# Kernel optimization log

Hardware: AMD Instinct MI355X
Metric: run time of the kernel (lower is better)

## Reference

```python
import jax, jax.numpy as jnp
import numpy as np

NHEAD = 16
HEAD_DIM = 64
ROPE_BASE = 10000.0


def _rotate_half(x):
    # interleaved convention: pairs (x0,x1)->(-x1,x0)
    x1 = x[..., ::2]
    x2 = x[..., 1::2]
    return jnp.stack([-x2, x1], axis=-1).reshape(x.shape)


def _rope_cache(seq_len, head_dim, base):
    half = head_dim // 2
    inv_freq = 1.0 / base ** (jnp.arange(half, dtype=jnp.float32) / float(half))
    t = jnp.arange(seq_len, dtype=jnp.float32)
    freqs = jnp.einsum('i,j->ij', t, inv_freq)          # [T, half]
    emb = jnp.concatenate([freqs, freqs], axis=-1)      # [T, D] (half-half cat, matches torch source)
    return jnp.cos(emb), jnp.sin(emb)


def setup_inputs() -> dict:
    key = jax.random.key(0)
    k1, k2, k3 = jax.random.split(key, 3)
    b, t, c = 2, 2048, 1024
    x = jax.random.normal(k1, (b, t, c), dtype=jnp.float32)
    # torch nn.Linear weights: [out_features, in_features], scaled like kaiming-uniform-ish
    W_qkv = jax.random.normal(k2, (3 * c, c), dtype=jnp.float32) / np.sqrt(c)
    W_out = jax.random.normal(k3, (c, c), dtype=jnp.float32) / np.sqrt(c)
    return {"x": x, "W_qkv": W_qkv, "W_out": W_out}


def reference(x, W_qkv, W_out):
    b, t, c = x.shape
    nh, hd = NHEAD, HEAD_DIM
    qkv = x @ W_qkv.T                                   # [b, t, 3c]
    q, k, v = jnp.split(qkv, 3, axis=-1)

    def to_heads(a):
        return a.reshape(b, t, nh, hd).transpose(0, 2, 1, 3)  # [b, nh, t, hd]

    q, k, v = to_heads(q), to_heads(k), to_heads(v)
    cos, sin = _rope_cache(t, hd, ROPE_BASE)            # [t, hd]
    cos = cos.astype(q.dtype)[None, None]
    sin = sin.astype(q.dtype)[None, None]
    q = q * cos + _rotate_half(q) * sin
    k = k * cos + _rotate_half(k) * sin

    scale = 1.0 / np.sqrt(hd).astype(np.float32)
    scores = jnp.einsum('bhqd,bhkd->bhqk', q, k) * scale
    attn = jax.nn.softmax(scores, axis=-1)
    y = jnp.einsum('bhqk,bhkd->bhqd', attn, v)          # [b, nh, t, hd]
    y = y.transpose(0, 2, 1, 3).reshape(b, t, c)
    return y @ W_out.T
```

## Files before the change

kernel.cpp:

```cpp
#include <hip/hip_runtime.h>
#include <hip/hip_bf16.h>
#include <math.h>

typedef __hip_bfloat16 bf16;
typedef _Float16 f16;
typedef __attribute__((ext_vector_type(8))) short bf16x8;
typedef __attribute__((ext_vector_type(8))) _Float16 f16x8;
typedef __attribute__((ext_vector_type(4))) float f32x4;
typedef __attribute__((ext_vector_type(4))) unsigned u32x4;

#define MFMA_BF(a,b,c) __builtin_amdgcn_mfma_f32_16x16x32_bf16((a),(b),(c),0,0,0)
#define MFMA_F16(a,b,c) __builtin_amdgcn_mfma_f32_16x16x32_f16((a),(b),(c),0,0,0)

__device__ __forceinline__ void load_lds16(const void* g, void* l) {
  __builtin_amdgcn_global_load_lds(
      (__attribute__((address_space(1))) void*)(g),
      (__attribute__((address_space(3))) void*)(l), 16, 0, 0);
}

__device__ __forceinline__ unsigned pk_bf16(float a, float b) {
  unsigned ua = __builtin_bit_cast(unsigned, a);
  unsigned ub = __builtin_bit_cast(unsigned, b);
  ua += 0x7fffu + ((ua >> 16) & 1u);
  ub += 0x7fffu + ((ub >> 16) & 1u);
  return (ua >> 16) | (ub & 0xffff0000u);
}

__device__ __forceinline__ unsigned cvtpk_bf16(float a, float b) {
  unsigned r;
  __asm__("v_cvt_pk_bf16_f32 %0, %1, %2" : "=v"(r) : "v"(a), "v"(b));
  return r;
}

__global__ void cvt_all(const float* __restrict__ x, const float* __restrict__ wq,
                        const float* __restrict__ wo, unsigned* __restrict__ xb,
                        unsigned* __restrict__ wqb, unsigned* __restrict__ wob) {
  int i = blockIdx.x * blockDim.x + threadIdx.x;
  const float* src;
  unsigned* dst;
  int off;
  if (i < 1048576) { src = x; dst = xb; off = i; }
  else if (i < 1048576 + 786432) { src = wq; dst = wqb; off = i - 1048576; }
  else { src = wo; dst = wob; off = i - (1048576 + 786432); }
  float4 v = reinterpret_cast<const float4*>(src)[off];
  uint2 u;
  u.x = cvtpk_bf16(v.x, v.y);
  u.y = cvtpk_bf16(v.z, v.w);
  reinterpret_cast<uint2*>(dst)[off] = u;
}

__global__ __launch_bounds__(256, 3)
void gemm_qkv(const bf16* __restrict__ A, const bf16* __restrict__ B,
              bf16* __restrict__ outq, bf16* __restrict__ outk,
              f16* __restrict__ outv) {
  __shared__ __align__(16) bf16 As[3][128 * 32];
  __shared__ __align__(16) bf16 Bs[3][128 * 32];
  const int K = 1024;
  const int tid = threadIdx.x;
  const int w = tid >> 6;
  const int lane = tid & 63;
  const int quad = lane >> 4;
  const int col = lane & 15;
  const int waveM = w >> 1;
  const int waveN = w & 1;
  const int bm = blockIdx.y * 128;
  const int bn = blockIdx.x * 128;

  f32x4 acc[4][4] = {};
  const int srow = lane >> 2;
  const int skoff = (((lane & 3) ^ ((srow >> 1) & 3))) * 8;
  const int swq = (quad ^ ((col >> 1) & 3)) * 8;

  auto stage = [&](int k0, int sb) {
#pragma unroll
    for (int p = 0; p < 2; ++p) {
      int r = p * 64 + w * 16 + srow;
      load_lds16(A + (size_t)(bm + r) * K + k0 + skoff,
                 (char*)As + sb * 8192 + p * 4096 + w * 1024);
      load_lds16(B + (size_t)(bn + r) * K + k0 + skoff,
                 (char*)Bs + sb * 8192 + p * 4096 + w * 1024);
    }
  };

  stage(0, 0);
  stage(32, 1);

  int cb = 0;
  for (int k0 = 0; k0 < K; k0 += 32) {
    if (k0 + 32 < K) __asm__ volatile("s_waitcnt vmcnt(4)" ::: "memory");
    else             __asm__ volatile("s_waitcnt vmcnt(0)" ::: "memory");
    __asm__ volatile("s_barrier" ::: "memory");
    if (k0 + 64 < K) {
      int nb = cb + 2; if (nb >= 3) nb -= 3;
      stage(k0 + 64, nb);
    }
    const bf16* at = &As[cb][0];
    const bf16* bt = &Bs[cb][0];
    bf16x8 af[4], bfr[4];
#pragma unroll
    for (int i = 0; i < 4; ++i)
      af[i] = *reinterpret_cast<const bf16x8*>(at + (waveM * 64 + i * 16 + col) * 32 + swq);
#pragma unroll
    for (int j = 0; j < 4; ++j)
      bfr[j] = *reinterpret_cast<const bf16x8*>(bt + (waveN * 64 + j * 16 + col) * 32 + swq);
#pragma unroll
    for (int i = 0; i < 4; ++i)
#pragma unroll
      for (int j = 0; j < 4; ++j)
        acc[i][j] = MFMA_BF(af[i], bfr[j], acc[i][j]);
    cb = (cb == 2) ? 0 : cb + 1;
  }

  if (bn < 2048) {
    const float NEGK = -0.4152410118f;
    const float C1 = 0.1803368799f;
    const float sgn = (col & 1) ? 1.0f : -1.0f;
#pragma unroll
    for (int j = 0; j < 4; ++j) {
      const int n0 = bn + waveN * 64 + j * 16;
      const int sel = n0 >> 10;
      const int hh = (n0 & 1023) >> 6;
      const int dd = (n0 & 63) + col;
      bf16* outp = sel ? outk : outq;
      const float post = sel ? 1.0f : C1;
      const float invf = __builtin_amdgcn_exp2f((float)((n0 & 31) + col) * NEGK);
#pragma unroll
      for (int i = 0; i < 4; ++i) {
#pragma unroll
        for (int r = 0; r < 4; ++r) {
          int m = bm + waveM * 64 + i * 16 + quad * 4 + r;
          int b = m >> 11, t = m & 2047;
          float v = acc[i][j][r];
          float partner = __shfl_xor(v, 1);
          float ang = (float)t * invf;
          float res = (v * __cosf(ang) + sgn * partner * __sinf(ang)) * post;
          outp[((size_t)(b * 16 + hh) * 2048 + t) * 64 + dd] = __float2bfloat16(res);
        }
      }
    }
  } else {
    const int b = bm >> 11;
    const int tt0 = (bm & 2047) + waveM * 64;
#pragma unroll
    for (int j = 0; j < 4; ++j) {
      const int n0 = bn + waveN * 64 + j * 16;
      const int hh = (n0 & 1023) >> 6;
      const int dd = (n0 & 63) + col;
      f16* dst = outv + (size_t)(b * 16 + hh) * 131072 + (size_t)dd * 2048;
#pragma unroll
      for (int i = 0; i < 4; ++i) {
        uint2 pk;
        pk.x = __builtin_bit_cast(unsigned, __builtin_amdgcn_cvt_pkrtz(acc[i][j][0], acc[i][j][1]));
        pk.y = __builtin_bit_cast(unsigned, __builtin_amdgcn_cvt_pkrtz(acc[i][j][2], acc[i][j][3]));
        *reinterpret_cast<uint2*>(dst + tt0 + i * 16 + quad * 4) = pk;
      }
    }
  }
}

__global__ __launch_bounds__(256, 4)
void gemm_out(const bf16* __restrict__ A, const bf16* __restrict__ B,
              float* __restrict__ outf) {
  __shared__ __align__(16) bf16 As[3][64 * 32];
  __shared__ __align__(16) bf16 Bs[3][64 * 32];
  const int K = 1024;
  const int tid = threadIdx.x;
  const int w = tid >> 6;
  const int lane = tid & 63;
  const int quad = lane >> 4;
  const int col = lane & 15;
  const int waveM = w >> 1;
  const int waveN = w & 1;
  const int bm = blockIdx.y * 64;
  const int bn = blockIdx.x * 64;

  f32x4 acc[2][2] = {};
  const int srow = lane >> 2;
  const int skoff = (((lane & 3) ^ ((srow >> 1) & 3))) * 8;
  const int swq = (quad ^ ((col >> 1) & 3)) * 8;

  auto stage = [&](int k0, int sb) {
    int r = w * 16 + srow;
    load_lds16(A + (size_t)(bm + r) * K + k0 + skoff,
               (char*)As + sb * 4096 + w * 1024);
    load_lds16(B + (size_t)(bn + r) * K + k0 + skoff,
               (char*)Bs + sb * 4096 + w * 1024);
  };

  stage(0, 0);
  stage(32, 1);

  int cb = 0;
  for (int k0 = 0; k0 < K; k0 += 32) {
    if (k0 + 32 < K) __asm__ volatile("s_waitcnt vmcnt(2)" ::: "memory");
    else             __asm__ volatile("s_waitcnt vmcnt(0)" ::: "memory");
    __asm__ volatile("s_barrier" ::: "memory");
    if (k0 + 64 < K) {
      int nb = cb + 2; if (nb >= 3) nb -= 3;
      stage(k0 + 64, nb);
    }
    const bf16* at = &As[cb][0];
    const bf16* bt = &Bs[cb][0];
    bf16x8 af[2], bfr[2];
#pragma unroll
    for (int i = 0; i < 2; ++i)
      af[i] = *reinterpret_cast<const bf16x8*>(at + (waveM * 32 + i * 16 + col) * 32 + swq);
#pragma unroll
    for (int j = 0; j < 2; ++j)
      bfr[j] = *reinterpret_cast<const bf16x8*>(bt + (waveN * 32 + j * 16 + col) * 32 + swq);
#pragma unroll
    for (int i = 0; i < 2; ++i)
#pragma unroll
      for (int j = 0; j < 2; ++j)
        acc[i][j] = MFMA_BF(af[i], bfr[j], acc[i][j]);
    cb = (cb == 2) ? 0 : cb + 1;
  }

#pragma unroll
  for (int i = 0; i < 2; ++i)
#pragma unroll
    for (int j = 0; j < 2; ++j) {
      const int n0 = bn + waveN * 32 + j * 16;
#pragma unroll
      for (int r = 0; r < 4; ++r) {
        int m = bm + waveM * 32 + i * 16 + quad * 4 + r;
        outf[(size_t)m * 1024 + n0 + col] = acc[i][j][r];
      }
    }
}

__global__ __launch_bounds__(256, 2)
void attn_kernel(const bf16* __restrict__ qh, const bf16* __restrict__ kh,
                 const f16* __restrict__ vt, bf16* __restrict__ y) {
  __shared__ __align__(16) bf16 Ks[2][2 * 64 * 64];
  __shared__ __align__(16) f16 Vs[3][2 * 64 * 64];

  const int bh = blockIdx.x;
  const int qt = blockIdx.y;
  const int w = threadIdx.x >> 6;
  const int lane = threadIdx.x & 63;
  const int quad = lane >> 4;
  const int col = lane & 15;

  const int qrow0 = qt * 128 + w * 32 + col;
  bf16x8 qf[2][2];
#pragma unroll
  for (int f = 0; f < 2; ++f)
#pragma unroll
    for (int c = 0; c < 2; ++c)
      qf[f][c] = *reinterpret_cast<const bf16x8*>(
          qh + ((size_t)bh * 2048 + qrow0 + f * 16) * 64 + c * 32 + quad * 8);

  const int s8 = lane >> 3;
  const int blk = (lane & 7) ^ s8;
  const bf16* kg = kh + (size_t)bh * 2048 * 64;
  const f16* vg = vt + (size_t)bh * 64 * 2048;
  const int ks0 = 32 * (w >> 1) + 8 * ((4 * w + (s8 >> 2)) & 3) + 4 * (w & 1) + (s8 & 3);
  const int ks1 = 32 * (w >> 1) + 8 * ((4 * w + 2 + (s8 >> 2)) & 3) + 4 * (w & 1) + (s8 & 3);
  const int vrow0 = w * 16 + s8;

  const int csw = col & 7;
  const int sw0 = (quad ^ csw) * 8;
  const int sw1 = ((quad + 4) ^ csw) * 8;
  const int rdbase = col * 64;

  f32x4 O[2][4] = {};
  float l[2] = {};
  f16x8 pf[2][4];

  auto stageK2 = [&](int kn, int kb) {
    char* kbp = (char*)Ks + kb * 16384 + w * 2048;
    load_lds16(kg + (size_t)(kn + ks0) * 64 + blk * 8, kbp);
    load_lds16(kg + (size_t)(kn + ks1) * 64 + blk * 8, kbp + 1024);
    load_lds16(kg + (size_t)(kn + 64 + ks0) * 64 + blk * 8, kbp + 8192);
    load_lds16(kg + (size_t)(kn + 64 + ks1) * 64 + blk * 8, kbp + 8192 + 1024);
  };
  auto stageV2 = [&](int kn, int vb) {
    char* vbp = (char*)Vs + vb * 16384 + w * 2048;
    load_lds16(vg + (size_t)vrow0 * 2048 + kn + blk * 8, vbp);
    load_lds16(vg + (size_t)(vrow0 + 8) * 2048 + kn + blk * 8, vbp + 1024);
    load_lds16(vg + (size_t)vrow0 * 2048 + kn + 64 + blk * 8, vbp + 8192);
    load_lds16(vg + (size_t)(vrow0 + 8) * 2048 + kn + 64 + blk * 8, vbp + 8192 + 1024);
  };

  auto softmax = [&](f32x4 (&s)[2][2][4]) {
#pragma unroll
    for (int f = 0; f < 2; ++f) {
      unsigned pk[16];
      float lf = 0.0f;
#pragma unroll
      for (int u = 0; u < 2; ++u)
#pragma unroll
        for (int t = 0; t < 4; ++t) {
          float p0 = __builtin_amdgcn_exp2f(s[f][u][t][0]);
          float p1 = __builtin_amdgcn_exp2f(s[f][u][t][1]);
          float p2 = __builtin_amdgcn_exp2f(s[f][u][t][2]);
          float p3 = __builtin_amdgcn_exp2f(s[f][u][t][3]);
          lf += (p0 + p1) + (p2 + p3);
          pk[u * 8 + t * 2]     = __builtin_bit_cast(unsigned, __builtin_amdgcn_cvt_pkrtz(p0, p1));
          pk[u * 8 + t * 2 + 1] = __builtin_bit_cast(unsigned, __builtin_amdgcn_cvt_pkrtz(p2, p3));
        }
      l[f] += lf;
      pf[f][0] = __builtin_bit_cast(f16x8, (u32x4){pk[0], pk[1], pk[2], pk[3]});
      pf[f][1] = __builtin_bit_cast(f16x8, (u32x4){pk[4], pk[5], pk[6], pk[7]});
      pf[f][2] = __builtin_bit_cast(f16x8, (u32x4){pk[8], pk[9], pk[10], pk[11]});
      pf[f][3] = __builtin_bit_cast(f16x8, (u32x4){pk[12], pk[13], pk[14], pk[15]});
    }
  };

  stageK2(0, 0);
  stageV2(0, 0);

  __asm__ volatile("s_waitcnt vmcnt(4)" ::: "memory");
  __asm__ volatile("s_barrier" ::: "memory");
  stageK2(128, 1);
  stageV2(128, 1);
  {
    f32x4 s[2][2][4];
    __builtin_amdgcn_s_setprio(1);
#pragma unroll
    for (int u = 0; u < 2; ++u) {
      const bf16* kt = &Ks[0][u * 4096];
#pragma unroll
      for (int t = 0; t < 4; ++t) {
        bf16x8 kf0 = *reinterpret_cast<const bf16x8*>(kt + t * 1024 + rdbase + sw0);
        bf16x8 kf1 = *reinterpret_cast<const bf16x8*>(kt + t * 1024 + rdbase + sw1);
#pragma unroll
        for (int f = 0; f < 2; ++f) {
          f32x4 a = {};
          a = MFMA_BF(kf0, qf[f][0], a);
          a = MFMA_BF(kf1, qf[f][1], a);
          s[f][u][t] = a;
        }
      }
    }
    __builtin_amdgcn_s_setprio(0);
    softmax(s);
  }

  int vprev = 0;
  int vnext = 2;
#pragma unroll 1
  for (int c = 1; c < 16; ++c) {
    const int kc = c * 128;
    __asm__ volatile("s_waitcnt vmcnt(4)" ::: "memory");
    __asm__ volatile("s_barrier" ::: "memory");
    if (c + 1 < 16) {
      stageK2(kc + 128, (c + 1) & 1);
      stageV2(kc + 128, vnext);
    }

    f32x4 s[2][2][4];
    __builtin_amdgcn_s_setprio(1);
#pragma unroll
    for (int u = 0; u < 2; ++u) {
      const bf16* kt = &Ks[c & 1][u * 4096];
      const f16* vtile = &Vs[vprev][u * 4096];
#pragma unroll
      for (int t = 0; t < 4; ++t) {
        bf16x8 kf0 = *reinterpret_cast<const bf16x8*>(kt + t * 1024 + rdbase + sw0);
        bf16x8 kf1 = *reinterpret_cast<const bf16x8*>(kt + t * 1024 + rdbase + sw1);
        f16x8 vf0 = *reinterpret_cast<const f16x8*>(vtile + t * 1024 + rdbase + sw0);
        f16x8 vf1 = *reinterpret_cast<const f16x8*>(vtile + t * 1024 + rdbase + sw1);
#pragma unroll
        for (int f = 0; f < 2; ++f) {
          f32x4 a = {};
          a = MFMA_BF(kf0, qf[f][0], a);
          a = MFMA_BF(kf1, qf[f][1], a);
          s[f][u][t] = a;
          O[f][t] = MFMA_F16(vf0, pf[f][u * 2], O[f][t]);
          O[f][t] = MFMA_F16(vf1, pf[f][u * 2 + 1], O[f][t]);
        }
      }
    }
    __builtin_amdgcn_s_setprio(0);
    softmax(s);

    vprev = (vprev == 2) ? 0 : vprev + 1;
    vnext = (vnext == 2) ? 0 : vnext + 1;
  }

  __asm__ volatile("s_waitcnt vmcnt(0)" ::: "memory");
  __asm__ volatile("s_barrier" ::: "memory");
  {
    __builtin_amdgcn_s_setprio(1);
#pragma unroll
    for (int u = 0; u < 2; ++u) {
      const f16* vtile = &Vs[vprev][u * 4096];
#pragma unroll
      for (int t = 0; t < 4; ++t) {
        f16x8 vf0 = *reinterpret_cast<const f16x8*>(vtile + t * 1024 + rdbase + sw0);
        f16x8 vf1 = *reinterpret_cast<const f16x8*>(vtile + t * 1024 + rdbase + sw1);
#pragma unroll
        for (int f = 0; f < 2; ++f) {
          O[f][t] = MFMA_F16(vf0, pf[f][u * 2], O[f][t]);
          O[f][t] = MFMA_F16(vf1, pf[f][u * 2 + 1], O[f][t]);
        }
      }
    }
    __builtin_amdgcn_s_setprio(0);
  }

  const int b = bh >> 4, h = bh & 15;
#pragma unroll
  for (int f = 0; f < 2; ++f) {
    float lv = l[f];
    lv += __shfl_xor(lv, 16, 64);
    lv += __shfl_xor(lv, 32, 64);
    float inv = 1.0f / lv;
    int tq = qt * 128 + w * 32 + f * 16 + col;
    size_t base = ((size_t)b * 2048 + tq) * 1024 + h * 64;
#pragma unroll
    for (int j = 0; j < 4; ++j) {
      uint2 pk2;
      pk2.x = pk_bf16(O[f][j][0] * inv, O[f][j][1] * inv);
      pk2.y = pk_bf16(O[f][j][2] * inv, O[f][j][3] * inv);
      *reinterpret_cast<uint2*>((unsigned short*)y + base + j * 16 + quad * 4) = pk2;
    }
  }
}

extern "C" void kernel_launch(void* const* d_in, const int* in_sizes, int n_in,
                              void* d_out, int out_size, void* d_ws, size_t ws_size,
                              hipStream_t stream) {
  const float* x    = (const float*)d_in[0];
  const float* wqkv = (const float*)d_in[1];
  const float* wout = (const float*)d_in[2];
  float* out = (float*)d_out;
  char* ws = (char*)d_ws;

  bf16* xb    = (bf16*)(ws);
  bf16* wqkvb = (bf16*)(ws + (size_t)(8 << 20));
  bf16* woutb = (bf16*)(ws + (size_t)(14 << 20));
  bf16* qh    = (bf16*)(ws + (size_t)(16 << 20));
  bf16* kh    = (bf16*)(ws + (size_t)(24 << 20));
  f16*  vt    = (f16*) (ws + (size_t)(32 << 20));
  bf16* y     = (bf16*)(ws);

  cvt_all<<<8192, 256, 0, stream>>>(x, wqkv, wout,
                                    (unsigned*)xb, (unsigned*)wqkvb, (unsigned*)woutb);
  gemm_qkv<<<dim3(24, 32), 256, 0, stream>>>(xb, wqkvb, qh, kh, vt);
  attn_kernel<<<dim3(32, 16), 256, 0, stream>>>(qh, kh, vt, y);
  gemm_out<<<dim3(16, 64), 256, 0, stream>>>(y, woutb, out);
}
```

Before: 172.9 us.

## Split K across two wave groups in output projection GEMM with LDS reduction

```diff
diff --git a/kernel.cpp b/kernel.cpp
--- a/kernel.cpp
+++ b/kernel.cpp
@@ -158,21 +158,25 @@
   }
 }
 
-__global__ __launch_bounds__(256, 4)
+__global__ __launch_bounds__(512, 4)
 void gemm_out(const bf16* __restrict__ A, const bf16* __restrict__ B,
               float* __restrict__ outf) {
-  __shared__ __align__(16) bf16 As[3][64 * 32];
-  __shared__ __align__(16) bf16 Bs[3][64 * 32];
+  __shared__ __align__(16) bf16 As[3][2][64 * 32];
+  __shared__ __align__(16) bf16 Bs[3][2][64 * 32];
+  __shared__ float Rs[64][65];
   const int K = 1024;
   const int tid = threadIdx.x;
   const int w = tid >> 6;
+  const int kh = w >> 2;
+  const int wl = w & 3;
   const int lane = tid & 63;
   const int quad = lane >> 4;
   const int col = lane & 15;
-  const int waveM = w >> 1;
-  const int waveN = w & 1;
+  const int waveM = wl >> 1;
+  const int waveN = wl & 1;
   const int bm = blockIdx.y * 64;
   const int bn = blockIdx.x * 64;
+  const int kbase = kh * 512;
 
   f32x4 acc[2][2] = {};
   const int srow = lane >> 2;
@@ -180,27 +184,27 @@
   const int swq = (quad ^ ((col >> 1) & 3)) * 8;
 
   auto stage = [&](int k0, int sb) {
-    int r = w * 16 + srow;
-    load_lds16(A + (size_t)(bm + r) * K + k0 + skoff,
-               (char*)As + sb * 4096 + w * 1024);
-    load_lds16(B + (size_t)(bn + r) * K + k0 + skoff,
-               (char*)Bs + sb * 4096 + w * 1024);
+    int r = wl * 16 + srow;
+    load_lds16(A + (size_t)(bm + r) * K + kbase + k0 + skoff,
+               (char*)As + (sb * 2 + kh) * 4096 + wl * 1024);
+    load_lds16(B + (size_t)(bn + r) * K + kbase + k0 + skoff,
+               (char*)Bs + (sb * 2 + kh) * 4096 + wl * 1024);
   };
 
   stage(0, 0);
   stage(32, 1);
 
   int cb = 0;
-  for (int k0 = 0; k0 < K; k0 += 32) {
-    if (k0 + 32 < K) __asm__ volatile("s_waitcnt vmcnt(2)" ::: "memory");
-    else             __asm__ volatile("s_waitcnt vmcnt(0)" ::: "memory");
+  for (int k0 = 0; k0 < 512; k0 += 32) {
+    if (k0 + 32 < 512) __asm__ volatile("s_waitcnt vmcnt(2)" ::: "memory");
+    else               __asm__ volatile("s_waitcnt vmcnt(0)" ::: "memory");
     __asm__ volatile("s_barrier" ::: "memory");
-    if (k0 + 64 < K) {
+    if (k0 + 64 < 512) {
       int nb = cb + 2; if (nb >= 3) nb -= 3;
       stage(k0 + 64, nb);
     }
-    const bf16* at = &As[cb][0];
-    const bf16* bt = &Bs[cb][0];
+    const bf16* at = &As[cb][kh][0];
+    const bf16* bt = &Bs[cb][kh][0];
     bf16x8 af[2], bfr[2];
 #pragma unroll
     for (int i = 0; i < 2; ++i)
@@ -216,17 +220,30 @@
     cb = (cb == 2) ? 0 : cb + 1;
   }
 
-#pragma unroll
-  for (int i = 0; i < 2; ++i)
-#pragma unroll
-    for (int j = 0; j < 2; ++j) {
-      const int n0 = bn + waveN * 32 + j * 16;
-#pragma unroll
-      for (int r = 0; r < 4; ++r) {
-        int m = bm + waveM * 32 + i * 16 + quad * 4 + r;
-        outf[(size_t)m * 1024 + n0 + col] = acc[i][j][r];
-      }
-    }
+  if (kh == 1) {
+#pragma unroll
+    for (int i = 0; i < 2; ++i)
+#pragma unroll
+      for (int j = 0; j < 2; ++j)
+#pragma unroll
+        for (int r = 0; r < 4; ++r)
+          Rs[waveM * 32 + i * 16 + quad * 4 + r][waveN * 32 + j * 16 + col] = acc[i][j][r];
+  }
+  __syncthreads();
+  if (kh == 0) {
+#pragma unroll
+    for (int i = 0; i < 2; ++i)
+#pragma unroll
+      for (int j = 0; j < 2; ++j) {
+        const int nl = waveN * 32 + j * 16;
+#pragma unroll
+        for (int r = 0; r < 4; ++r) {
+          const int ml = waveM * 32 + i * 16 + quad * 4 + r;
+          outf[(size_t)(bm + ml) * 1024 + bn + nl + col] =
+              acc[i][j][r] + Rs[ml][nl + col];
+        }
+      }
+  }
 }
 
 __global__ __launch_bounds__(256, 2)
@@ -441,5 +458,5 @@
                                     (unsigned*)xb, (unsigned*)wqkvb, (unsigned*)woutb);
   gemm_qkv<<<dim3(24, 32), 256, 0, stream>>>(xb, wqkvb, qh, kh, vt);
   attn_kernel<<<dim3(32, 16), 256, 0, stream>>>(qh, kh, vt, y);
-  gemm_out<<<dim3(16, 64), 256, 0, stream>>>(y, woutb, out);
-}
+  gemm_out<<<dim3(16, 64), 512, 0, stream>>>(y, woutb, out);
+}
```

Result: no change. 172.7 us, median of 2 (-0.1%).
